# Optimization experiments

Hardware: AMD Instinct MI355X
Metric: run time of the kernel (lower is better)

## Reference

```python
import math
import jax, jax.numpy as jnp
import numpy as np

EPS = 1e-06
NB_FEATURES = 256
NUM_HEADS = 16


def fwht(x):
    """Fast Walsh-Hadamard transform along last dim (power-of-two size)."""
    shape = x.shape
    P = shape[-1]
    h = 1
    while h < P:
        x = x.reshape(shape[:-1] + (-1, 2 * h))
        a, b = x[..., :h], x[..., h:]
        x = jnp.concatenate([a + b, a - b], axis=-1).reshape(shape)
        h *= 2
    return x


def apply_rope(q, k):
    # q,k: (C,H,L,D); RoPE applied to tokens 1..L-1, token 0 (condition) skipped
    C, H, L, D = q.shape
    dtype = q.dtype
    freqs = 10000.0 ** (-jnp.arange(0, D, 2, dtype=dtype) / D)  # (D/2,)
    pos = jnp.arange(L - 1, dtype=dtype)[:, None]               # (L-1,1)
    ang = pos * freqs                                            # (L-1,D/2)
    cos, sin = jnp.cos(ang), jnp.sin(ang)

    def rot(t):
        ts = t[..., 1:, :]
        t1, t2 = ts[..., 0::2], ts[..., 1::2]
        re = t1 * cos - t2 * sin
        im = t1 * sin + t2 * cos
        rs = jnp.stack([re, im], axis=-1).reshape(ts.shape)  # re-interleave even/odd
        return jnp.concatenate([t[..., :1, :], rs], axis=-2)

    return rot(q), rot(k)


def sorf_phi(x, signs, scales, m):
    # x: (C,H,L,D); signs: (H,R,3,P); scales: (H,R,P)
    C, H, L, D = x.shape
    R, P = signs.shape[1], signs.shape[-1]
    x_p = x if D == P else jnp.pad(x, ((0, 0), (0, 0), (0, 0), (0, P - D)))
    inv = 1.0 / math.sqrt(P)
    s1 = signs[None, :, :, 0, None, :]  # (1,H,R,1,P)
    s2 = signs[None, :, :, 1, None, :]
    s3 = signs[None, :, :, 2, None, :]
    g = (scales * inv)[None, :, :, None, :]  # (1,H,R,1,P)
    t = fwht(x_p[:, :, None, :, :] * s1) * inv  # (C,H,R,L,P)
    t = fwht(t * s2) * inv
    t = fwht(t * s3) * inv
    block = t * g
    phi = block.transpose(0, 1, 3, 2, 4).reshape(C, H, L, R * P)[..., :m]
    x_norm_sq = jnp.sum(x * x, axis=-1, keepdims=True) / 2.0
    return jnp.exp(phi - x_norm_sq) / math.sqrt(m)


def setup_inputs() -> dict:
    key = jax.random.key(0)
    ks = jax.random.split(key, 5)
    C, L, E = 4, 4096, 1024
    H, D = NUM_HEADS, 1024 // NUM_HEADS  # D = 64
    P = 64  # next power of two >= D
    R = 4   # ceil(256 / 64)
    x = jax.random.normal(ks[0], (C, L, E), dtype=jnp.float32)
    w_qkv = jax.random.normal(ks[1], (3 * E, E), dtype=jnp.float32) / math.sqrt(E)
    w_out = jax.random.normal(ks[2], (E, E), dtype=jnp.float32) / math.sqrt(E)
    sorf_signs = (2.0 * jax.random.randint(ks[3], (H, R, 3, P), 0, 2) - 1.0).astype(jnp.float32)
    sorf_scales = jax.random.normal(ks[4], (H, R, P), dtype=jnp.float32)
    return {"x": x, "w_qkv": w_qkv, "w_out": w_out,
            "sorf_signs": sorf_signs, "sorf_scales": sorf_scales}


def reference(x, w_qkv, w_out, sorf_signs, sorf_scales):
    C, L, E = x.shape
    H = NUM_HEADS
    D = E // H
    qkv = x @ w_qkv.T  # (C,L,3E)
    q, k, v = jnp.split(qkv, 3, axis=-1)
    to_heads = lambda t: t.reshape(C, L, H, D).transpose(0, 2, 1, 3)  # (C,H,L,D)
    q, k, v = to_heads(q), to_heads(k), to_heads(v)
    q, k = apply_rope(q, k)
    q_phi = sorf_phi(q, sorf_signs, sorf_scales, NB_FEATURES)  # (C,H,L,m)
    k_phi = sorf_phi(k, sorf_signs, sorf_scales, NB_FEATURES)
    # non-causal linear attention aggregation
    S = jnp.einsum('chlm,chld->chmd', k_phi, v)       # (C,H,m,D)
    sum_k = jnp.sum(k_phi, axis=2)                    # (C,H,m)
    numer = jnp.einsum('chlm,chmd->chld', q_phi, S)   # (C,H,L,D)
    denom = jnp.maximum(jnp.einsum('chlm,chm->chl', q_phi, sum_k), EPS)
    out_heads = numer / denom[..., None]
    out = out_heads.transpose(0, 2, 1, 3).reshape(C, L, E)
    return out @ w_out.T
```

## Files before the change

kernel.cpp:

```cpp
#include <hip/hip_runtime.h>
#include <math.h>


#define LOG2_10000 13.287712379549449f
#define TCONST 15.201805f
#define SIGMA 0.0009765625f

typedef __attribute__((ext_vector_type(8))) _Float16 h8;
typedef __attribute__((ext_vector_type(4))) _Float16 h4;
typedef __attribute__((ext_vector_type(4))) float f32x4;

#define GLDS16(gptr, lptr) __builtin_amdgcn_global_load_lds( \
    (const __attribute__((address_space(1))) void*)(gptr),   \
    (__attribute__((address_space(3))) void*)(lptr), 16, 0, 0)

__global__ __launch_bounds__(256) void k_zero(float* __restrict__ p, size_t n) {
    size_t i = (size_t)blockIdx.x * 256 + threadIdx.x;
    const size_t st = (size_t)gridDim.x * 256;
    for (; i < n; i += st) p[i] = 0.0f;
}

__global__ __launch_bounds__(256) void k_cvt_xw(const float* __restrict__ x,
                                                const float* __restrict__ wqkv,
                                                const float* __restrict__ wout,
                                                _Float16* __restrict__ xh,
                                                _Float16* __restrict__ wh,
                                                _Float16* __restrict__ wob) {
    const size_t st = (size_t)gridDim.x * 256;
    const size_t nx = (size_t)16384 * 1024 / 4;
    for (size_t i = (size_t)blockIdx.x * 256 + threadIdx.x; i < nx; i += st) {
        float4 v = ((const float4*)x)[i];
        h4 o = {(_Float16)v.x, (_Float16)v.y, (_Float16)v.z, (_Float16)v.w};
        ((h4*)xh)[i] = o;
    }
    const size_t nw = (size_t)3072 * 1024 / 4;
    for (size_t i = (size_t)blockIdx.x * 256 + threadIdx.x; i < nw; i += st) {
        float4 v = ((const float4*)wqkv)[i];
        h4 o = {(_Float16)v.x, (_Float16)v.y, (_Float16)v.z, (_Float16)v.w};
        ((h4*)wh)[i] = o;
    }
    const size_t no = (size_t)1024 * 1024 / 4;
    for (size_t i = (size_t)blockIdx.x * 256 + threadIdx.x; i < no; i += st) {
        float4 v = ((const float4*)wout)[i];
        h4 o = {(_Float16)v.x, (_Float16)v.y, (_Float16)v.z, (_Float16)v.w};
        ((h4*)wob)[i] = o;
    }
}

__global__ __launch_bounds__(64) void k_build_atf(const float* __restrict__ signs,
                                                  const float* __restrict__ scales,
                                                  _Float16* __restrict__ atfG) {
    const int b = blockIdx.x;
    const int hh = b >> 2, r = b & 3;
    const int j = threadIdx.x;
    const float* s1 = signs + ((size_t)(hh * 4 + r) * 3 + 0) * 64;
    const float* s2 = s1 + 64;
    const float* s3 = s1 + 128;
    const float* sc = scales + (size_t)(hh * 4 + r) * 64;

    float v[64];
    const float s1j = s1[j];
#pragma unroll
    for (int p = 0; p < 64; ++p) v[p] = (p == j) ? s1j : 0.0f;
#pragma unroll
    for (int st = 1; st < 64; st <<= 1)
#pragma unroll
        for (int p = 0; p < 64; ++p)
            if (!(p & st)) { float a = v[p], bq = v[p | st]; v[p] = a + bq; v[p | st] = a - bq; }
#pragma unroll
    for (int p = 0; p < 64; ++p) v[p] *= s2[p];
#pragma unroll
    for (int st = 1; st < 64; st <<= 1)
#pragma unroll
        for (int p = 0; p < 64; ++p)
            if (!(p & st)) { float a = v[p], bq = v[p | st]; v[p] = a + bq; v[p | st] = a - bq; }
#pragma unroll
    for (int p = 0; p < 64; ++p) v[p] *= s3[p];
#pragma unroll
    for (int st = 1; st < 64; st <<= 1)
#pragma unroll
        for (int p = 0; p < 64; ++p)
            if (!(p & st)) { float a = v[p], bq = v[p | st]; v[p] = a + bq; v[p | st] = a - bq; }
#pragma unroll
    for (int p = 0; p < 64; ++p)
        atfG[((size_t)hh * 256 + r * 64 + p) * 64 + j] = (_Float16)(v[p] * sc[p] * (1.0f / 4096.0f));
}

__global__ __launch_bounds__(256) void k_qkv_f16(const _Float16* __restrict__ xh,
                                                 const _Float16* __restrict__ wh,
                                                 _Float16* __restrict__ qb,
                                                 _Float16* __restrict__ kb,
                                                 _Float16* __restrict__ vb,
                                                 float* __restrict__ nq,
                                                 float* __restrict__ nk,
                                                 int n_base, int nbn) {
    __shared__ char smem[65536];
    _Float16* Ol = (_Float16*)smem;

    const int tid = threadIdx.x;
    const int lane = tid & 63, w = tid >> 6;
    const int lane16 = lane & 15, lrow = lane >> 4;
    const int wm = w >> 1, wn = w & 1;

    const int per = gridDim.x >> 3;
    const int sw = ((int)blockIdx.x & 7) * per + ((int)blockIdx.x >> 3);
    const int bn = sw % nbn, bm = sw / nbn;
    const int m0 = bm * 128, n0 = n_base + bn * 128;

    f32x4 acc[4][4];
    const f32x4 zz = {0.f, 0.f, 0.f, 0.f};
#pragma unroll
    for (int i = 0; i < 4; ++i)
#pragma unroll
        for (int j = 0; j < 4; ++j) acc[i][j] = zz;

    {
        _Float16* Ad = (_Float16*)smem;
        _Float16* Bd = (_Float16*)smem + 16384;
#pragma unroll
        for (int s = 0; s < 4; ++s) {
            const int g = s * 256 + tid;
            const int row = g & 127, ks = g >> 7;
            GLDS16(xh + (size_t)(m0 + row) * 1024 + ks * 8, Ad + g * 8);
            GLDS16(wh + (size_t)(n0 + row) * 1024 + ks * 8, Bd + g * 8);
        }
    }
    __syncthreads();

    int cur = 0;
    for (int it = 0; it < 16; ++it) {
        if (it < 15) {
            const int kt = (it + 1) * 64;
            _Float16* Ad = (_Float16*)smem + (cur ^ 1) * 8192;
            _Float16* Bd = (_Float16*)smem + 16384 + (cur ^ 1) * 8192;
#pragma unroll
            for (int s = 0; s < 4; ++s) {
                const int g = s * 256 + tid;
                const int row = g & 127, ks = g >> 7;
                GLDS16(xh + (size_t)(m0 + row) * 1024 + kt + ks * 8, Ad + g * 8);
                GLDS16(wh + (size_t)(n0 + row) * 1024 + kt + ks * 8, Bd + g * 8);
            }
        }
        const _Float16* Ah = (_Float16*)smem + cur * 8192;
        const _Float16* Bh = (_Float16*)smem + 16384 + cur * 8192;
#pragma unroll
        for (int s = 0; s < 2; ++s) {
            const int kd = s * 4 + lrow;
            h8 af[4], bf[4];
#pragma unroll
            for (int i = 0; i < 4; ++i)
                af[i] = *(const h8*)(Ah + (kd * 128 + wm * 64 + i * 16 + lane16) * 8);
#pragma unroll
            for (int j = 0; j < 4; ++j)
                bf[j] = *(const h8*)(Bh + (kd * 128 + wn * 64 + j * 16 + lane16) * 8);
#pragma unroll
            for (int i = 0; i < 4; ++i)
#pragma unroll
                for (int j = 0; j < 4; ++j)
                    acc[i][j] = __builtin_amdgcn_mfma_f32_16x16x32_f16(af[i], bf[j], acc[i][j], 0, 0, 0);
        }
        __syncthreads();
        cur ^= 1;
    }

    const int sec = n0 >> 10;
    float freqj[4];
#pragma unroll
    for (int j = 0; j < 4; ++j) {
        const int colw = wn * 64 + j * 16 + lane16;
        freqj[j] = exp2f(-(float)((colw & 63) & ~1) * (LOG2_10000 / 64.0f));
    }

#pragma unroll
    for (int i = 0; i < 4; ++i) {
        float nsum[4] = {0.f, 0.f, 0.f, 0.f};
#pragma unroll
        for (int j = 0; j < 4; ++j) {
            const int colw = wn * 64 + j * 16 + lane16;
#pragma unroll
            for (int r = 0; r < 4; ++r) {
                float v = acc[i][j][r];
                const float partner = __shfl_xor(v, 1);
                const int gm = m0 + wm * 64 + i * 16 + lrow * 4 + r;
                const int l = gm & 4095;
                if (sec < 2 && l > 0) {
                    float sn, cs;
                    sincosf((float)(l - 1) * freqj[j], &sn, &cs);
                    v = v * cs + sn * ((lane & 1) ? partner : -partner);
                }
                const _Float16 hv = (_Float16)v;
                if (sec < 2) {
                    const float vr = (float)hv;
                    nsum[r] += vr * vr;
                }
                Ol[(wm * 64 + i * 16 + lrow * 4 + r) * 136 + colw] = hv;
            }
        }
        if (sec < 2) {
#pragma unroll
            for (int m = 1; m < 16; m <<= 1)
#pragma unroll
                for (int r = 0; r < 4; ++r) nsum[r] += __shfl_xor(nsum[r], m);
            if (lane16 == 0) {
                float* ntgt = (sec == 0) ? nq : nk;
                const int hh = ((unsigned)(n0 + wn * 64) >> 6) & 15;
#pragma unroll
                for (int r = 0; r < 4; ++r) {
                    const int gm = m0 + wm * 64 + i * 16 + lrow * 4 + r;
                    const int c = gm >> 12, l = gm & 4095;
                    ntgt[((size_t)(c * 16 + hh)) * 4096 + l] = 0.5f * nsum[r];
                }
            }
        }
    }
    __syncthreads();
    {
        const int row = tid >> 1, half = tid & 1;
        const int gm = m0 + row;
        const int c = gm >> 12, l = gm & 4095;
        const int hh = ((unsigned)(n0 + half * 64) >> 6) & 15;
        _Float16* tgt = (sec == 0) ? qb : (sec == 1) ? kb : vb;
        const size_t base = ((size_t)(c * 16 + hh) * 4096 + l) * 64;
#pragma unroll
        for (int q8 = 0; q8 < 8; ++q8)
            *(h8*)(tgt + base + q8 * 8) = *(h8*)(Ol + row * 136 + half * 64 + q8 * 8);
    }
}

__global__ __launch_bounds__(256) void k_minred(const float* __restrict__ nk,
                                                float* __restrict__ MG) {
    const int ch = blockIdx.x;
    const int tid = threadIdx.x;
    __shared__ float red[4];
    float v = 1e30f;
    for (int i = tid; i < 4096; i += 256) v = fminf(v, nk[(size_t)ch * 4096 + i]);
#pragma unroll
    for (int off = 32; off >= 1; off >>= 1) v = fminf(v, __shfl_down(v, off));
    if ((tid & 63) == 0) red[tid >> 6] = v;
    __syncthreads();
    if (tid == 0) MG[ch] = fminf(fminf(red[0], red[1]), fminf(red[2], red[3]));
}

__global__ __launch_bounds__(256) void k_kvstats(const _Float16* __restrict__ kb,
                                                 const _Float16* __restrict__ vb,
                                                 const float* __restrict__ nkG,
                                                 const _Float16* __restrict__ atfG,
                                                 const float* __restrict__ MG,
                                                 float* __restrict__ St,
                                                 float* __restrict__ sumk) {
    __shared__ char smem[29824];
    _Float16* kl = (_Float16*)smem;
    _Float16* vt = kl + 2048;
    _Float16* pt = vt + 2560;
    float* nks = (float*)(pt + 10240);

    const int tid = threadIdx.x;
    const int lane = tid & 63, w = tid >> 6;
    const int lane16 = lane & 15, lrow = lane >> 4;
    const int ch = blockIdx.x, split = blockIdx.y;
    const int h = ch & 15;
    const _Float16* atfH = atfG + (size_t)h * 16384;
    const float Mch = MG[ch];

    f32x4 Sacc[4][4];
    const f32x4 zz = {0.f, 0.f, 0.f, 0.f};
#pragma unroll
    for (int i = 0; i < 4; ++i)
#pragma unroll
        for (int j = 0; j < 4; ++j) Sacc[i][j] = zz;
    float skr[4][4] = {};

    for (int chunk = 0; chunk < 16; ++chunk) {
        const int l0 = split * 512 + chunk * 32;
        __syncthreads();
        {
            const int g = w * 64 + lane;
            GLDS16(kb + ((size_t)ch * 4096 + l0 + (g & 31)) * 64 + (g >> 5) * 8, kl + g * 8);
        }
        {
            const int l = tid >> 3, d0 = (tid & 7) * 8;
            const h8 vv = *(const h8*)(vb + ((size_t)ch * 4096 + l0 + l) * 64 + d0);
#pragma unroll
            for (int j = 0; j < 8; ++j) vt[(d0 + j) * 40 + l] = vv[j];
        }
        if (tid < 32) nks[tid] = nkG[(size_t)ch * 4096 + l0 + tid];
        __syncthreads();
        f32x4 p[4][2];
#pragma unroll
        for (int i = 0; i < 4; ++i) { p[i][0] = zz; p[i][1] = zz; }
#pragma unroll
        for (int ks = 0; ks < 2; ++ks) {
            const int kd = ks * 4 + lrow;
            h8 bfr[2];
#pragma unroll
            for (int nf = 0; nf < 2; ++nf)
                bfr[nf] = *(h8*)(kl + (kd * 32 + nf * 16 + lane16) * 8);
#pragma unroll
            for (int mf = 0; mf < 4; ++mf) {
                const int f = w * 64 + mf * 16 + lane16;
                const h8 a = *(const h8*)(atfH + (size_t)f * 64 + kd * 8);
#pragma unroll
                for (int nf = 0; nf < 2; ++nf)
                    p[mf][nf] = __builtin_amdgcn_mfma_f32_16x16x32_f16(a, bfr[nf], p[mf][nf], 0, 0, 0);
            }
        }
#pragma unroll
        for (int mf = 0; mf < 4; ++mf)
#pragma unroll
            for (int nf = 0; nf < 2; ++nf) {
                const int ll = nf * 16 + lane16;
                const float nv = nks[ll];
#pragma unroll
                for (int r = 0; r < 4; ++r) {
                    const float e = expf(p[mf][nf][r] - nv + Mch);
                    skr[mf][r] += e;
                    const int fr = w * 64 + mf * 16 + lrow * 4 + r;
                    pt[fr * 40 + ll] = (_Float16)e;
                }
            }
        __syncthreads();
        h8 bfr2[4];
#pragma unroll
        for (int nf = 0; nf < 4; ++nf)
            bfr2[nf] = *(h8*)(pt + (w * 64 + nf * 16 + lane16) * 40 + lrow * 8);
#pragma unroll
        for (int mf = 0; mf < 4; ++mf) {
            const h8 a = *(h8*)(vt + (mf * 16 + lane16) * 40 + lrow * 8);
#pragma unroll
            for (int nf = 0; nf < 4; ++nf)
                Sacc[mf][nf] = __builtin_amdgcn_mfma_f32_16x16x32_f16(a, bfr2[nf], Sacc[mf][nf], 0, 0, 0);
        }
    }
#pragma unroll
    for (int mf = 0; mf < 4; ++mf)
#pragma unroll
        for (int nf = 0; nf < 4; ++nf)
#pragma unroll
            for (int r = 0; r < 4; ++r) {
                const int d = mf * 16 + lrow * 4 + r;
                const int f = w * 64 + nf * 16 + lane16;
                atomicAdd(&St[((size_t)ch * 64 + d) * 256 + f], Sacc[mf][nf][r]);
            }
#pragma unroll
    for (int mf = 0; mf < 4; ++mf) {
#pragma unroll
        for (int m = 1; m < 16; m <<= 1)
#pragma unroll
            for (int r = 0; r < 4; ++r) skr[mf][r] += __shfl_xor(skr[mf][r], m);
        if (lane16 == 0)
#pragma unroll
            for (int r = 0; r < 4; ++r)
                atomicAdd(&sumk[(size_t)ch * 256 + w * 64 + mf * 16 + lrow * 4 + r], skr[mf][r]);
    }
}

__global__ __launch_bounds__(256) void k_cvt_st(const float* __restrict__ St,
                                                const float* __restrict__ sumk,
                                                _Float16* __restrict__ Stb) {
    const size_t n = (size_t)64 * 80 * 256;
    const size_t st = (size_t)gridDim.x * 256;
    for (size_t e = (size_t)blockIdx.x * 256 + threadIdx.x; e < n; e += st) {
        const int f = (int)(e & 255);
        const int row = (int)((e >> 8) % 80);
        const int ch = (int)(e / (80 * 256));
        float v = 0.0f;
        if (row < 64) v = St[((size_t)ch * 64 + row) * 256 + f];
        else if (row == 64) v = sumk[(size_t)ch * 256 + f];
        Stb[e] = (_Float16)(v * SIGMA);
    }
}

__global__ __launch_bounds__(256) void k_attn(const _Float16* __restrict__ qb,
                                              const float* __restrict__ nqG,
                                              const _Float16* __restrict__ atfG,
                                              const _Float16* __restrict__ Stb,
                                              const float* __restrict__ MG,
                                              _Float16* __restrict__ oh) {
    __shared__ char smem[41216];
    _Float16* pq = (_Float16*)smem;
    _Float16* ql = pq + 16384;
    float* nqs = (float*)(ql + 4096);
    _Float16* olds = pq;

    const int tid = threadIdx.x;
    const int lane = tid & 63, w = tid >> 6;
    const int lane16 = lane & 15, lrow = lane >> 4;
    const int ch = blockIdx.x, lb = blockIdx.y;
    const int h = ch & 15, c = ch >> 4;
    const int l0 = lb * 64;
    const _Float16* atfH = atfG + (size_t)h * 16384;
    const _Float16* stbH = Stb + (size_t)ch * 20480;
    const float Mch = MG[ch];

#pragma unroll
    for (int j = 0; j < 2; ++j) {
        const int g = (w * 2 + j) * 64 + lane;
        GLDS16(qb + ((size_t)ch * 4096 + l0 + (g & 63)) * 64 + (g >> 6) * 8, ql + g * 8);
    }
    if (tid < 64) nqs[tid] = nqG[(size_t)ch * 4096 + l0 + tid];
    __syncthreads();

    const f32x4 zz = {0.f, 0.f, 0.f, 0.f};
    {
        f32x4 p[16];
#pragma unroll
        for (int nf = 0; nf < 16; ++nf) p[nf] = zz;
#pragma unroll
        for (int ks = 0; ks < 2; ++ks) {
            const int kd = ks * 4 + lrow;
            const h8 a = *(h8*)(ql + (kd * 64 + w * 16 + lane16) * 8);
#pragma unroll
            for (int nf = 0; nf < 16; ++nf) {
                const int f = nf * 16 + lane16;
                const h8 b = *(const h8*)(atfH + (size_t)f * 64 + kd * 8);
                p[nf] = __builtin_amdgcn_mfma_f32_16x16x32_f16(a, b, p[nf], 0, 0, 0);
            }
        }
#pragma unroll
        for (int nf = 0; nf < 16; ++nf) {
            const int f = nf * 16 + lane16;
#pragma unroll
            for (int r = 0; r < 4; ++r) {
                const float e = expf(p[nf][r]);
                const int l = w * 16 + lrow * 4 + r;
                pq[((f >> 3) * 64 + l) * 8 + (f & 7)] = (_Float16)e;
            }
        }
    }
    __syncthreads();
    f32x4 nacc[5];
#pragma unroll
    for (int nf = 0; nf < 5; ++nf) nacc[nf] = zz;
#pragma unroll
    for (int ks = 0; ks < 8; ++ks) {
        const int kd = ks * 4 + lrow;
        const h8 a = *(h8*)(pq + (kd * 64 + w * 16 + lane16) * 8);
#pragma unroll
        for (int nf = 0; nf < 5; ++nf) {
            const int dd = nf * 16 + lane16;
            const h8 b = *(const h8*)(stbH + (size_t)dd * 256 + kd * 8);
            nacc[nf] = __builtin_amdgcn_mfma_f32_16x16x32_f16(a, b, nacc[nf], 0, 0, 0);
        }
    }
    __syncthreads();
    {
#pragma unroll
        for (int r = 0; r < 4; ++r) {
            const float dn = __shfl(nacc[4][r], (lane & 48));
            const int row = w * 16 + lrow * 4 + r;
            const float t = expf(nqs[row] + Mch - TCONST);
            const float rden = 1.0f / fmaxf(dn, t);
#pragma unroll
            for (int nf = 0; nf < 4; ++nf)
                olds[row * 72 + nf * 16 + lane16] = (_Float16)(nacc[nf][r] * rden);
        }
    }
    __syncthreads();
    {
        const int row = tid >> 2, d0 = (tid & 3) * 16;
        const size_t base = ((size_t)c * 4096 + l0 + row) * 1024 + h * 64 + d0;
        *(h8*)(oh + base) = *(h8*)(olds + row * 72 + d0);
        *(h8*)(oh + base + 8) = *(h8*)(olds + row * 72 + d0 + 8);
    }
}

__global__ __launch_bounds__(256) void k_outgemm(const _Float16* __restrict__ OH,
                                                 const _Float16* __restrict__ WOB,
                                                 float* __restrict__ OUT) {
    __shared__ char smem[65536];

    const int tid = threadIdx.x;
    const int lane = tid & 63, w = tid >> 6;
    const int lane16 = lane & 15, lrow = lane >> 4;
    const int wm = w >> 1, wn = w & 1;

    const int per = gridDim.x >> 3;
    const int sw = ((int)blockIdx.x & 7) * per + ((int)blockIdx.x >> 3);
    const int bn = sw & 7, bm = sw >> 3;
    const int m0 = bm * 128, n0 = bn * 128;

    f32x4 acc[4][4];
    const f32x4 zz = {0.f, 0.f, 0.f, 0.f};
#pragma unroll
    for (int i = 0; i < 4; ++i)
#pragma unroll
        for (int j = 0; j < 4; ++j) acc[i][j] = zz;

    {
        _Float16* Ad = (_Float16*)smem;
        _Float16* Bd = (_Float16*)smem + 16384;
#pragma unroll
        for (int s = 0; s < 4; ++s) {
            const int g = s * 256 + tid;
            const int row = g & 127, ks = g >> 7;
            GLDS16(OH + (size_t)(m0 + row) * 1024 + ks * 8, Ad + g * 8);
            GLDS16(WOB + (size_t)(n0 + row) * 1024 + ks * 8, Bd + g * 8);
        }
    }
    __syncthreads();

    int cur = 0;
    for (int it = 0; it < 16; ++it) {
        if (it < 15) {
            const int kt = (it + 1) * 64;
            _Float16* Ad = (_Float16*)smem + (cur ^ 1) * 8192;
            _Float16* Bd = (_Float16*)smem + 16384 + (cur ^ 1) * 8192;
#pragma unroll
            for (int s = 0; s < 4; ++s) {
                const int g = s * 256 + tid;
                const int row = g & 127, ks = g >> 7;
                GLDS16(OH + (size_t)(m0 + row) * 1024 + kt + ks * 8, Ad + g * 8);
                GLDS16(WOB + (size_t)(n0 + row) * 1024 + kt + ks * 8, Bd + g * 8);
            }
        }
        const _Float16* Ah = (_Float16*)smem + cur * 8192;
        const _Float16* Bh = (_Float16*)smem + 16384 + cur * 8192;
#pragma unroll
        for (int s = 0; s < 2; ++s) {
            const int kd = s * 4 + lrow;
            h8 af[4], bf[4];
#pragma unroll
            for (int i = 0; i < 4; ++i)
                af[i] = *(const h8*)(Ah + (kd * 128 + wm * 64 + i * 16 + lane16) * 8);
#pragma unroll
            for (int j = 0; j < 4; ++j)
                bf[j] = *(const h8*)(Bh + (kd * 128 + wn * 64 + j * 16 + lane16) * 8);
#pragma unroll
            for (int i = 0; i < 4; ++i)
#pragma unroll
                for (int j = 0; j < 4; ++j)
                    acc[i][j] = __builtin_amdgcn_mfma_f32_16x16x32_f16(af[i], bf[j], acc[i][j], 0, 0, 0);
        }
        __syncthreads();
        cur ^= 1;
    }
#pragma unroll
    for (int i = 0; i < 4; ++i)
#pragma unroll
        for (int j = 0; j < 4; ++j)
#pragma unroll
            for (int r = 0; r < 4; ++r) {
                const int gm = m0 + wm * 64 + i * 16 + lrow * 4 + r;
                const int gn = n0 + wn * 64 + j * 16 + lane16;
                OUT[(size_t)gm * 1024 + gn] = acc[i][j][r];
            }
}

extern "C" void kernel_launch(void* const* d_in, const int* in_sizes, int n_in,
                              void* d_out, int out_size, void* d_ws, size_t ws_size,
                              hipStream_t stream) {
    const float* x      = (const float*)d_in[0];
    const float* w_qkv  = (const float*)d_in[1];
    const float* w_out  = (const float*)d_in[2];
    const float* signs  = (const float*)d_in[3];
    const float* scales = (const float*)d_in[4];
    float* out = (float*)d_out;

    _Float16* hs = (_Float16*)d_ws;
    _Float16* xh  = hs;
    _Float16* wh  = xh + 16777216;
    _Float16* wob = wh + 3145728;
    _Float16* kb  = wob + 1048576;
    _Float16* vb  = kb + 16777216;
    _Float16* atf = vb + 16777216;
    _Float16* stb = atf + 262144;
    float* St   = (float*)(stb + 1310720);
    float* sumk = St + 1048576;
    float* nq   = sumk + 16384;
    float* nk   = nq + 262144;
    float* MG   = nk + 262144;
    _Float16* qb = kb;
    _Float16* oh = vb;

    k_cvt_xw<<<dim3(1024), dim3(256), 0, stream>>>(x, w_qkv, w_out, xh, wh, wob);
    k_build_atf<<<dim3(64), dim3(64), 0, stream>>>(signs, scales, atf);
    k_zero<<<dim3(1024), dim3(256), 0, stream>>>(St, (size_t)1048576 + 16384);
    k_qkv_f16<<<dim3(2048), dim3(256), 0, stream>>>(xh, wh, qb, kb, vb, nq, nk, 1024, 16);
    k_minred<<<dim3(64), dim3(256), 0, stream>>>(nk, MG);
    k_kvstats<<<dim3(64, 8), dim3(256), 0, stream>>>(kb, vb, nk, atf, MG, St, sumk);
    k_cvt_st<<<dim3(1280), dim3(256), 0, stream>>>(St, sumk, stb);
    k_qkv_f16<<<dim3(1024), dim3(256), 0, stream>>>(xh, wh, qb, kb, vb, nq, nk, 0, 8);
    k_attn<<<dim3(64, 64), dim3(256), 0, stream>>>(qb, nq, atf, stb, MG, oh);
    k_outgemm<<<dim3(1024), dim3(256), 0, stream>>>(oh, wob, out);
}
```

Before: 709.3 us.

## Merge small kernels, double-buffer kvstats, use fast sincos, coalesce qkv stores

Combines the conversion, zeroing and ATF-build kernels into one launch, folds the min-reduction into kvstats, and runs the Stb conversion alongside the Q GEMM in one kernel. This cuts launch count from ten to six. kvstats now double-buffers its K/V chunk loads, and RoPE switches to a hardware sin/cos with manual range reduction. QKV output stores are reordered for coalescing and nq/nk values are read directly into registers. Risks are lower sincos precision, and each kvstats split block now redundantly recomputes the per-channel min and writes it to MG.

New measurement: 661.4 us. 6.8% less time.

```diff
diff --git a/kernel.cpp b/kernel.cpp
--- a/kernel.cpp
+++ b/kernel.cpp
@@ -5,6 +5,8 @@
 #define LOG2_10000 13.287712379549449f
 #define TCONST 15.201805f
 #define SIGMA 0.0009765625f
+#define INV2PI 0.15915494309189535f
+#define INV2PI_ERR 6.4206383e-9f
 
 typedef __attribute__((ext_vector_type(8))) _Float16 h8;
 typedef __attribute__((ext_vector_type(4))) _Float16 h4;
@@ -14,96 +16,103 @@
     (const __attribute__((address_space(1))) void*)(gptr),   \
     (__attribute__((address_space(3))) void*)(lptr), 16, 0, 0)
 
-__global__ __launch_bounds__(256) void k_zero(float* __restrict__ p, size_t n) {
-    size_t i = (size_t)blockIdx.x * 256 + threadIdx.x;
-    const size_t st = (size_t)gridDim.x * 256;
-    for (; i < n; i += st) p[i] = 0.0f;
-}
-
-__global__ __launch_bounds__(256) void k_cvt_xw(const float* __restrict__ x,
-                                                const float* __restrict__ wqkv,
-                                                const float* __restrict__ wout,
-                                                _Float16* __restrict__ xh,
-                                                _Float16* __restrict__ wh,
-                                                _Float16* __restrict__ wob) {
-    const size_t st = (size_t)gridDim.x * 256;
-    const size_t nx = (size_t)16384 * 1024 / 4;
-    for (size_t i = (size_t)blockIdx.x * 256 + threadIdx.x; i < nx; i += st) {
-        float4 v = ((const float4*)x)[i];
-        h4 o = {(_Float16)v.x, (_Float16)v.y, (_Float16)v.z, (_Float16)v.w};
-        ((h4*)xh)[i] = o;
-    }
-    const size_t nw = (size_t)3072 * 1024 / 4;
-    for (size_t i = (size_t)blockIdx.x * 256 + threadIdx.x; i < nw; i += st) {
-        float4 v = ((const float4*)wqkv)[i];
-        h4 o = {(_Float16)v.x, (_Float16)v.y, (_Float16)v.z, (_Float16)v.w};
-        ((h4*)wh)[i] = o;
-    }
-    const size_t no = (size_t)1024 * 1024 / 4;
-    for (size_t i = (size_t)blockIdx.x * 256 + threadIdx.x; i < no; i += st) {
-        float4 v = ((const float4*)wout)[i];
-        h4 o = {(_Float16)v.x, (_Float16)v.y, (_Float16)v.z, (_Float16)v.w};
-        ((h4*)wob)[i] = o;
-    }
-}
-
-__global__ __launch_bounds__(64) void k_build_atf(const float* __restrict__ signs,
-                                                  const float* __restrict__ scales,
-                                                  _Float16* __restrict__ atfG) {
-    const int b = blockIdx.x;
-    const int hh = b >> 2, r = b & 3;
-    const int j = threadIdx.x;
-    const float* s1 = signs + ((size_t)(hh * 4 + r) * 3 + 0) * 64;
-    const float* s2 = s1 + 64;
-    const float* s3 = s1 + 128;
-    const float* sc = scales + (size_t)(hh * 4 + r) * 64;
-
-    float v[64];
-    const float s1j = s1[j];
-#pragma unroll
-    for (int p = 0; p < 64; ++p) v[p] = (p == j) ? s1j : 0.0f;
-#pragma unroll
-    for (int st = 1; st < 64; st <<= 1)
+static __device__ __forceinline__ void fast_sincos(float ang, float* sn, float* cs) {
+    const float t = ang * INV2PI;
+    const float k = floorf(t);
+    float r = fmaf(ang, INV2PI, -k);
+    r = fmaf(ang, INV2PI_ERR, r);
+    *sn = __builtin_amdgcn_sinf(r);
+    *cs = __builtin_amdgcn_cosf(r);
+}
+
+__global__ __launch_bounds__(256) void k_pre(const float* __restrict__ x,
+                                             const float* __restrict__ wqkv,
+                                             const float* __restrict__ wout,
+                                             _Float16* __restrict__ xh,
+                                             _Float16* __restrict__ wh,
+                                             _Float16* __restrict__ wob,
+                                             float* __restrict__ zbase,
+                                             const float* __restrict__ signs,
+                                             const float* __restrict__ scales,
+                                             _Float16* __restrict__ atfG) {
+    const int bid = blockIdx.x;
+    const int tid = threadIdx.x;
+    if (bid < 2048) {
+        const size_t st = (size_t)2048 * 256;
+        const size_t nx = (size_t)16384 * 1024 / 4;
+        for (size_t i = (size_t)bid * 256 + tid; i < nx; i += st) {
+            float4 v = ((const float4*)x)[i];
+            h4 o = {(_Float16)v.x, (_Float16)v.y, (_Float16)v.z, (_Float16)v.w};
+            ((h4*)xh)[i] = o;
+        }
+        const size_t nw = (size_t)3072 * 1024 / 4;
+        for (size_t i = (size_t)bid * 256 + tid; i < nw; i += st) {
+            float4 v = ((const float4*)wqkv)[i];
+            h4 o = {(_Float16)v.x, (_Float16)v.y, (_Float16)v.z, (_Float16)v.w};
+            ((h4*)wh)[i] = o;
+        }
+        const size_t no = (size_t)1024 * 1024 / 4;
+        for (size_t i = (size_t)bid * 256 + tid; i < no; i += st) {
+            float4 v = ((const float4*)wout)[i];
+            h4 o = {(_Float16)v.x, (_Float16)v.y, (_Float16)v.z, (_Float16)v.w};
+            ((h4*)wob)[i] = o;
+        }
+        const size_t nz = (size_t)1048576 + 16384;
+        for (size_t i = (size_t)bid * 256 + tid; i < nz; i += st) zbase[i] = 0.0f;
+    } else if (tid < 64) {
+        const int b = bid - 2048;
+        const int hh = b >> 2, r = b & 3;
+        const int j = tid;
+        const float* s1 = signs + ((size_t)(hh * 4 + r) * 3 + 0) * 64;
+        const float* s2 = s1 + 64;
+        const float* s3 = s1 + 128;
+        const float* sc = scales + (size_t)(hh * 4 + r) * 64;
+        float v[64];
+        const float s1j = s1[j];
+#pragma unroll
+        for (int p = 0; p < 64; ++p) v[p] = (p == j) ? s1j : 0.0f;
+#pragma unroll
+        for (int st2 = 1; st2 < 64; st2 <<= 1)
+#pragma unroll
+            for (int p = 0; p < 64; ++p)
+                if (!(p & st2)) { float a = v[p], bq = v[p | st2]; v[p] = a + bq; v[p | st2] = a - bq; }
+#pragma unroll
+        for (int p = 0; p < 64; ++p) v[p] *= s2[p];
+#pragma unroll
+        for (int st2 = 1; st2 < 64; st2 <<= 1)
+#pragma unroll
+            for (int p = 0; p < 64; ++p)
+                if (!(p & st2)) { float a = v[p], bq = v[p | st2]; v[p] = a + bq; v[p | st2] = a - bq; }
+#pragma unroll
+        for (int p = 0; p < 64; ++p) v[p] *= s3[p];
+#pragma unroll
+        for (int st2 = 1; st2 < 64; st2 <<= 1)
+#pragma unroll
+            for (int p = 0; p < 64; ++p)
+                if (!(p & st2)) { float a = v[p], bq = v[p | st2]; v[p] = a + bq; v[p | st2] = a - bq; }
 #pragma unroll
         for (int p = 0; p < 64; ++p)
-            if (!(p & st)) { float a = v[p], bq = v[p | st]; v[p] = a + bq; v[p | st] = a - bq; }
-#pragma unroll
-    for (int p = 0; p < 64; ++p) v[p] *= s2[p];
-#pragma unroll
-    for (int st = 1; st < 64; st <<= 1)
-#pragma unroll
-        for (int p = 0; p < 64; ++p)
-            if (!(p & st)) { float a = v[p], bq = v[p | st]; v[p] = a + bq; v[p | st] = a - bq; }
-#pragma unroll
-    for (int p = 0; p < 64; ++p) v[p] *= s3[p];
-#pragma unroll
-    for (int st = 1; st < 64; st <<= 1)
-#pragma unroll
-        for (int p = 0; p < 64; ++p)
-            if (!(p & st)) { float a = v[p], bq = v[p | st]; v[p] = a + bq; v[p | st] = a - bq; }
-#pragma unroll
-    for (int p = 0; p < 64; ++p)
-        atfG[((size_t)hh * 256 + r * 64 + p) * 64 + j] = (_Float16)(v[p] * sc[p] * (1.0f / 4096.0f));
-}
-
-__global__ __launch_bounds__(256) void k_qkv_f16(const _Float16* __restrict__ xh,
-                                                 const _Float16* __restrict__ wh,
-                                                 _Float16* __restrict__ qb,
-                                                 _Float16* __restrict__ kb,
-                                                 _Float16* __restrict__ vb,
-                                                 float* __restrict__ nq,
-                                                 float* __restrict__ nk,
-                                                 int n_base, int nbn) {
-    __shared__ char smem[65536];
+            atfG[((size_t)hh * 256 + r * 64 + p) * 64 + j] = (_Float16)(v[p] * sc[p] * (1.0f / 4096.0f));
+    }
+}
+
+static __device__ __forceinline__ void qkv_body(char* smem,
+                                                const _Float16* __restrict__ xh,
+                                                const _Float16* __restrict__ wh,
+                                                _Float16* __restrict__ qb,
+                                                _Float16* __restrict__ kb,
+                                                _Float16* __restrict__ vb,
+                                                float* __restrict__ nq,
+                                                float* __restrict__ nk,
+                                                int swid, int n_base, int nbn, int nwg) {
     _Float16* Ol = (_Float16*)smem;
-
     const int tid = threadIdx.x;
     const int lane = tid & 63, w = tid >> 6;
     const int lane16 = lane & 15, lrow = lane >> 4;
     const int wm = w >> 1, wn = w & 1;
 
-    const int per = gridDim.x >> 3;
-    const int sw = ((int)blockIdx.x & 7) * per + ((int)blockIdx.x >> 3);
+    const int per = nwg >> 3;
+    const int sw = (swid & 7) * per + (swid >> 3);
     const int bn = sw % nbn, bm = sw / nbn;
     const int m0 = bm * 128, n0 = n_base + bn * 128;
 
@@ -185,7 +194,7 @@
                 const int l = gm & 4095;
                 if (sec < 2 && l > 0) {
                     float sn, cs;
-                    sincosf((float)(l - 1) * freqj[j], &sn, &cs);
+                    fast_sincos((float)(l - 1) * freqj[j], &sn, &cs);
                     v = v * cs + sn * ((lane & 1) ? partner : -partner);
                 }
                 const _Float16 hv = (_Float16)v;
@@ -215,44 +224,46 @@
     }
     __syncthreads();
     {
-        const int row = tid >> 1, half = tid & 1;
-        const int gm = m0 + row;
-        const int c = gm >> 12, l = gm & 4095;
-        const int hh = ((unsigned)(n0 + half * 64) >> 6) & 15;
         _Float16* tgt = (sec == 0) ? qb : (sec == 1) ? kb : vb;
-        const size_t base = ((size_t)(c * 16 + hh) * 4096 + l) * 64;
-#pragma unroll
-        for (int q8 = 0; q8 < 8; ++q8)
-            *(h8*)(tgt + base + q8 * 8) = *(h8*)(Ol + row * 136 + half * 64 + q8 * 8);
-    }
-}
-
-__global__ __launch_bounds__(256) void k_minred(const float* __restrict__ nk,
-                                                float* __restrict__ MG) {
-    const int ch = blockIdx.x;
-    const int tid = threadIdx.x;
-    __shared__ float red[4];
-    float v = 1e30f;
-    for (int i = tid; i < 4096; i += 256) v = fminf(v, nk[(size_t)ch * 4096 + i]);
-#pragma unroll
-    for (int off = 32; off >= 1; off >>= 1) v = fminf(v, __shfl_down(v, off));
-    if ((tid & 63) == 0) red[tid >> 6] = v;
-    __syncthreads();
-    if (tid == 0) MG[ch] = fminf(fminf(red[0], red[1]), fminf(red[2], red[3]));
+#pragma unroll
+        for (int t2 = 0; t2 < 8; ++t2) {
+            const int g = t2 * 256 + tid;
+            const int half = g >> 10, r = (g >> 3) & 127, d8 = g & 7;
+            const int gm = m0 + r;
+            const int c = gm >> 12, l = gm & 4095;
+            const int hh = ((unsigned)(n0 + half * 64) >> 6) & 15;
+            const size_t base = ((size_t)(c * 16 + hh) * 4096 + l) * 64 + d8 * 8;
+            *(h8*)(tgt + base) = *(h8*)(Ol + r * 136 + half * 64 + d8 * 8);
+        }
+    }
+}
+
+__global__ __launch_bounds__(256) void k_qkv_f16(const _Float16* __restrict__ xh,
+                                                 const _Float16* __restrict__ wh,
+                                                 _Float16* __restrict__ qb,
+                                                 _Float16* __restrict__ kb,
+                                                 _Float16* __restrict__ vb,
+                                                 float* __restrict__ nq,
+                                                 float* __restrict__ nk,
+                                                 int n_base, int nbn, int nwg) {
+    __shared__ char smem[65536];
+    qkv_body(smem, xh, wh, qb, kb, vb, nq, nk, (int)blockIdx.x, n_base, nbn, nwg);
 }
 
 __global__ __launch_bounds__(256) void k_kvstats(const _Float16* __restrict__ kb,
                                                  const _Float16* __restrict__ vb,
                                                  const float* __restrict__ nkG,
                                                  const _Float16* __restrict__ atfG,
-                                                 const float* __restrict__ MG,
+                                                 float* __restrict__ MG,
                                                  float* __restrict__ St,
                                                  float* __restrict__ sumk) {
-    __shared__ char smem[29824];
-    _Float16* kl = (_Float16*)smem;
-    _Float16* vt = kl + 2048;
-    _Float16* pt = vt + 2560;
-    float* nks = (float*)(pt + 10240);
+    __shared__ char smem[38944];
+    _Float16* kl0 = (_Float16*)smem;
+    _Float16* kl1 = kl0 + 2048;
+    _Float16* vt0 = kl1 + 2048;
+    _Float16* vt1 = vt0 + 2560;
+    _Float16* pt  = vt1 + 2560;
+    float* red = (float*)(pt + 10240);
 
     const int tid = threadIdx.x;
     const int lane = tid & 63, w = tid >> 6;
@@ -260,7 +271,16 @@
     const int ch = blockIdx.x, split = blockIdx.y;
     const int h = ch & 15;
     const _Float16* atfH = atfG + (size_t)h * 16384;
-    const float Mch = MG[ch];
+    const int lv = tid >> 3, d0v = (tid & 7) * 8;
+
+    float mv = 1e30f;
+    for (int i = tid; i < 4096; i += 256) mv = fminf(mv, nkG[(size_t)ch * 4096 + i]);
+#pragma unroll
+    for (int off = 32; off >= 1; off >>= 1) mv = fminf(mv, __shfl_xor(mv, off));
+    if (lane == 0) red[w] = mv;
+    __syncthreads();
+    const float Mch = fminf(fminf(red[0], red[1]), fminf(red[2], red[3]));
+    if (tid == 0) MG[ch] = Mch;
 
     f32x4 Sacc[4][4];
     const f32x4 zz = {0.f, 0.f, 0.f, 0.f};
@@ -270,21 +290,30 @@
         for (int j = 0; j < 4; ++j) Sacc[i][j] = zz;
     float skr[4][4] = {};
 
+    {
+        const int g = w * 64 + lane;
+        GLDS16(kb + ((size_t)ch * 4096 + split * 512 + (g & 31)) * 64 + (g >> 5) * 8, kl0 + g * 8);
+    }
+    h8 vreg = *(const h8*)(vb + ((size_t)ch * 4096 + split * 512 + lv) * 64 + d0v);
+    __syncthreads();
+#pragma unroll
+    for (int j = 0; j < 8; ++j) vt0[(d0v + j) * 40 + lv] = vreg[j];
+
     for (int chunk = 0; chunk < 16; ++chunk) {
+        const int cur = chunk & 1;
         const int l0 = split * 512 + chunk * 32;
-        __syncthreads();
-        {
+        _Float16* klc = cur ? kl1 : kl0;
+        _Float16* kln = cur ? kl0 : kl1;
+        _Float16* vtc = cur ? vt1 : vt0;
+        _Float16* vtn = cur ? vt0 : vt1;
+        if (chunk < 15) {
+            const int l0n = l0 + 32;
             const int g = w * 64 + lane;
-            GLDS16(kb + ((size_t)ch * 4096 + l0 + (g & 31)) * 64 + (g >> 5) * 8, kl + g * 8);
-        }
-        {
-            const int l = tid >> 3, d0 = (tid & 7) * 8;
-            const h8 vv = *(const h8*)(vb + ((size_t)ch * 4096 + l0 + l) * 64 + d0);
-#pragma unroll
-            for (int j = 0; j < 8; ++j) vt[(d0 + j) * 40 + l] = vv[j];
-        }
-        if (tid < 32) nks[tid] = nkG[(size_t)ch * 4096 + l0 + tid];
-        __syncthreads();
+            GLDS16(kb + ((size_t)ch * 4096 + l0n + (g & 31)) * 64 + (g >> 5) * 8, kln + g * 8);
+            vreg = *(const h8*)(vb + ((size_t)ch * 4096 + l0n + lv) * 64 + d0v);
+        }
+        const float nv0 = nkG[(size_t)ch * 4096 + l0 + lane16];
+        const float nv1 = nkG[(size_t)ch * 4096 + l0 + 16 + lane16];
         f32x4 p[4][2];
 #pragma unroll
         for (int i = 0; i < 4; ++i) { p[i][0] = zz; p[i][1] = zz; }
@@ -294,7 +323,7 @@
             h8 bfr[2];
 #pragma unroll
             for (int nf = 0; nf < 2; ++nf)
-                bfr[nf] = *(h8*)(kl + (kd * 32 + nf * 16 + lane16) * 8);
+                bfr[nf] = *(h8*)(klc + (kd * 32 + nf * 16 + lane16) * 8);
 #pragma unroll
             for (int mf = 0; mf < 4; ++mf) {
                 const int f = w * 64 + mf * 16 + lane16;
@@ -309,10 +338,10 @@
 #pragma unroll
             for (int nf = 0; nf < 2; ++nf) {
                 const int ll = nf * 16 + lane16;
-                const float nv = nks[ll];
+                const float nvv = nf ? nv1 : nv0;
 #pragma unroll
                 for (int r = 0; r < 4; ++r) {
-                    const float e = expf(p[mf][nf][r] - nv + Mch);
+                    const float e = expf(p[mf][nf][r] - nvv + Mch);
                     skr[mf][r] += e;
                     const int fr = w * 64 + mf * 16 + lrow * 4 + r;
                     pt[fr * 40 + ll] = (_Float16)e;
@@ -325,11 +354,16 @@
             bfr2[nf] = *(h8*)(pt + (w * 64 + nf * 16 + lane16) * 40 + lrow * 8);
 #pragma unroll
         for (int mf = 0; mf < 4; ++mf) {
-            const h8 a = *(h8*)(vt + (mf * 16 + lane16) * 40 + lrow * 8);
+            const h8 a = *(h8*)(vtc + (mf * 16 + lane16) * 40 + lrow * 8);
 #pragma unroll
             for (int nf = 0; nf < 4; ++nf)
                 Sacc[mf][nf] = __builtin_amdgcn_mfma_f32_16x16x32_f16(a, bfr2[nf], Sacc[mf][nf], 0, 0, 0);
         }
+        if (chunk < 15) {
+#pragma unroll
+            for (int j = 0; j < 8; ++j) vtn[(d0v + j) * 40 + lv] = vreg[j];
+        }
+        __syncthreads();
     }
 #pragma unroll
     for (int mf = 0; mf < 4; ++mf)
@@ -354,19 +388,32 @@
     }
 }
 
-__global__ __launch_bounds__(256) void k_cvt_st(const float* __restrict__ St,
-                                                const float* __restrict__ sumk,
-                                                _Float16* __restrict__ Stb) {
-    const size_t n = (size_t)64 * 80 * 256;
-    const size_t st = (size_t)gridDim.x * 256;
-    for (size_t e = (size_t)blockIdx.x * 256 + threadIdx.x; e < n; e += st) {
-        const int f = (int)(e & 255);
-        const int row = (int)((e >> 8) % 80);
-        const int ch = (int)(e / (80 * 256));
-        float v = 0.0f;
-        if (row < 64) v = St[((size_t)ch * 64 + row) * 256 + f];
-        else if (row == 64) v = sumk[(size_t)ch * 256 + f];
-        Stb[e] = (_Float16)(v * SIGMA);
+__global__ __launch_bounds__(256) void k_mid(const _Float16* __restrict__ xh,
+                                             const _Float16* __restrict__ wh,
+                                             _Float16* __restrict__ qb,
+                                             _Float16* __restrict__ kb,
+                                             _Float16* __restrict__ vb,
+                                             float* __restrict__ nq,
+                                             float* __restrict__ nk,
+                                             const float* __restrict__ St,
+                                             const float* __restrict__ sumk,
+                                             _Float16* __restrict__ Stb) {
+    __shared__ char smem[65536];
+    const int bid = blockIdx.x;
+    if (bid < 1024) {
+        qkv_body(smem, xh, wh, qb, kb, vb, nq, nk, bid, 0, 8, 1024);
+    } else {
+        const size_t n = (size_t)64 * 80 * 256;
+        const size_t st = (size_t)256 * 256;
+        for (size_t e = (size_t)(bid - 1024) * 256 + threadIdx.x; e < n; e += st) {
+            const int f = (int)(e & 255);
+            const int row = (int)((e >> 8) % 80);
+            const int ch = (int)(e / (80 * 256));
+            float v = 0.0f;
+            if (row < 64) v = St[((size_t)ch * 64 + row) * 256 + f];
+            else if (row == 64) v = sumk[(size_t)ch * 256 + f];
+            Stb[e] = (_Float16)(v * SIGMA);
+        }
     }
 }
 
@@ -376,10 +423,9 @@
                                               const _Float16* __restrict__ Stb,
                                               const float* __restrict__ MG,
                                               _Float16* __restrict__ oh) {
-    __shared__ char smem[41216];
+    __shared__ char smem[40960];
     _Float16* pq = (_Float16*)smem;
     _Float16* ql = pq + 16384;
-    float* nqs = (float*)(ql + 4096);
     _Float16* olds = pq;
 
     const int tid = threadIdx.x;
@@ -397,7 +443,10 @@
         const int g = (w * 2 + j) * 64 + lane;
         GLDS16(qb + ((size_t)ch * 4096 + l0 + (g & 63)) * 64 + (g >> 6) * 8, ql + g * 8);
     }
-    if (tid < 64) nqs[tid] = nqG[(size_t)ch * 4096 + l0 + tid];
+    float nv[4];
+#pragma unroll
+    for (int r = 0; r < 4; ++r)
+        nv[r] = nqG[(size_t)ch * 4096 + l0 + w * 16 + lrow * 4 + r];
     __syncthreads();
 
     const f32x4 zz = {0.f, 0.f, 0.f, 0.f};
@@ -448,7 +497,7 @@
         for (int r = 0; r < 4; ++r) {
             const float dn = __shfl(nacc[4][r], (lane & 48));
             const int row = w * 16 + lrow * 4 + r;
-            const float t = expf(nqs[row] + Mch - TCONST);
+            const float t = expf(nv[r] + Mch - TCONST);
             const float rden = 1.0f / fmaxf(dn, t);
 #pragma unroll
             for (int nf = 0; nf < 4; ++nf)
@@ -468,7 +517,6 @@
                                                  const _Float16* __restrict__ WOB,
                                                  float* __restrict__ OUT) {
     __shared__ char smem[65536];
-
     const int tid = threadIdx.x;
     const int lane = tid & 63, w = tid >> 6;
     const int lane16 = lane & 15, lrow = lane >> 4;
@@ -572,14 +620,11 @@
     _Float16* qb = kb;
     _Float16* oh = vb;
 
-    k_cvt_xw<<<dim3(1024), dim3(256), 0, stream>>>(x, w_qkv, w_out, xh, wh, wob);
-    k_build_atf<<<dim3(64), dim3(64), 0, stream>>>(signs, scales, atf);
-    k_zero<<<dim3(1024), dim3(256), 0, stream>>>(St, (size_t)1048576 + 16384);
-    k_qkv_f16<<<dim3(2048), dim3(256), 0, stream>>>(xh, wh, qb, kb, vb, nq, nk, 1024, 16);
-    k_minred<<<dim3(64), dim3(256), 0, stream>>>(nk, MG);
+    k_pre<<<dim3(2112), dim3(256), 0, stream>>>(x, w_qkv, w_out, xh, wh, wob, St,
+                                                signs, scales, atf);
+    k_qkv_f16<<<dim3(2048), dim3(256), 0, stream>>>(xh, wh, qb, kb, vb, nq, nk, 1024, 16, 2048);
     k_kvstats<<<dim3(64, 8), dim3(256), 0, stream>>>(kb, vb, nk, atf, MG, St, sumk);
-    k_cvt_st<<<dim3(1280), dim3(256), 0, stream>>>(St, sumk, stb);
-    k_qkv_f16<<<dim3(1024), dim3(256), 0, stream>>>(xh, wh, qb, kb, vb, nq, nk, 0, 8);
+    k_mid<<<dim3(1280), dim3(256), 0, stream>>>(xh, wh, qb, kb, vb, nq, nk, St, sumk, stb);
     k_attn<<<dim3(64, 64), dim3(256), 0, stream>>>(qb, nq, atf, stb, MG, oh);
     k_outgemm<<<dim3(1024), dim3(256), 0, stream>>>(oh, wob, out);
 }
```
